# Optimization experiments

Measured on AMD Instinct MI355X. Metric: run time of the kernel, lower is better.

The kernel has to match this reference:

```python
import jax, jax.numpy as jnp
import numpy as np

L = 2048; V = 50000; E = 256
H1 = 512; H2 = 512; H3 = 512; H4 = 512
T = 11; START = 9; STOP = 10; ALPHA = 0.2
NEG = -10000.0


def setup_inputs() -> dict:
    key = jax.random.key(0)
    ks = jax.random.split(key, 25)
    def n(k, shape, s=0.05):
        return jax.random.normal(k, shape, dtype=jnp.float32) * s
    h1 = H1 // 2; h2 = H4 // 2
    trans = jax.random.normal(ks[23], (T, T), dtype=jnp.float32)
    trans = trans.at[START, :].set(NEG).at[:, STOP].set(NEG)
    return {
        "sentence": jax.random.randint(ks[0], (L,), 0, V),
        "emb": n(ks[1], (V, E), 0.1),
        "l1_wih_f": n(ks[2], (4 * h1, E)), "l1_whh_f": n(ks[3], (4 * h1, h1)), "l1_b_f": n(ks[4], (4 * h1,)),
        "l1_wih_b": n(ks[5], (4 * h1, E)), "l1_whh_b": n(ks[6], (4 * h1, h1)), "l1_b_b": n(ks[7], (4 * h1,)),
        "hc1": n(ks[8], (4, h1)),
        "gat1_W": n(ks[9], (H1, H2)), "gat1_a": n(ks[10], (2 * H2,)),
        "gat2_W": n(ks[11], (H2, H3)), "gat2_a": n(ks[12], (2 * H3,)),
        "l2_wih_f": n(ks[13], (4 * h2, H3)), "l2_whh_f": n(ks[14], (4 * h2, h2)), "l2_b_f": n(ks[15], (4 * h2,)),
        "l2_wih_b": n(ks[16], (4 * h2, H3)), "l2_whh_b": n(ks[17], (4 * h2, h2)), "l2_b_b": n(ks[18], (4 * h2,)),
        "hc2": n(ks[19], (4, h2)),
        "w_tag": n(ks[20], (T, H4)), "b_tag": n(ks[21], (T,)),
        "trans": trans,
    }


def _lstm_dir(x, h0, c0, wih, whh, b):
    # x: [L, D]; PyTorch gate order i, f, g, o
    def step(carry, xt):
        h, c = carry
        z = xt @ wih.T + h @ whh.T + b
        i, f, g, o = jnp.split(z, 4)
        i = jax.nn.sigmoid(i); f = jax.nn.sigmoid(f)
        g = jnp.tanh(g); o = jax.nn.sigmoid(o)
        c = f * c + i * g
        h = o * jnp.tanh(c)
        return (h, c), h
    _, hs = jax.lax.scan(step, (h0, c0), x)
    return hs


def _bilstm(x, wf, uf, bf, wb, ub, bb, hc):
    hf = _lstm_dir(x, hc[0], hc[1], wf, uf, bf)
    hb = _lstm_dir(x[::-1], hc[2], hc[3], wb, ub, bb)[::-1]
    return jnp.concatenate([hf, hb], axis=-1)  # [L, 2h]


def _gat(h, W, a):
    # dense GAT layer: attention over all node pairs (inference, no dropout)
    Wh = h @ W                                   # [L, F]
    F = W.shape[1]
    e = jax.nn.leaky_relu((Wh @ a[:F])[:, None] + (Wh @ a[F:])[None, :], ALPHA)  # [L, L]
    attn = jax.nn.softmax(e, axis=1)
    return attn @ Wh


def _viterbi(feats, trans):
    init = jnp.full((T,), NEG, dtype=feats.dtype).at[START].set(0.0)
    def step(fv, feat):
        scores = fv[None, :] + trans             # [next_tag, prev_tag]
        bp = jnp.argmax(scores, axis=1)
        fv2 = jnp.max(scores, axis=1) + feat
        return fv2, bp
    fv, bps = jax.lax.scan(step, init, feats)    # bps: [L, T]
    term = fv + trans[STOP]
    best = jnp.argmax(term)
    score = term[best]
    def back(tag, bp):
        return bp[tag], tag
    _, path = jax.lax.scan(back, best, bps, reverse=True)
    return score, path


def reference(sentence, emb, l1_wih_f, l1_whh_f, l1_b_f, l1_wih_b, l1_whh_b, l1_b_b, hc1,
              gat1_W, gat1_a, gat2_W, gat2_a,
              l2_wih_f, l2_whh_f, l2_b_f, l2_wih_b, l2_whh_b, l2_b_b, hc2,
              w_tag, b_tag, trans):
    x = emb[sentence]                                                  # [L, E]
    h1 = _bilstm(x, l1_wih_f, l1_whh_f, l1_b_f, l1_wih_b, l1_whh_b, l1_b_b, hc1)
    g1 = jax.nn.elu(_gat(h1, gat1_W, gat1_a))
    g2 = jax.nn.elu(_gat(g1, gat2_W, gat2_a))
    h2 = _bilstm(g2, l2_wih_f, l2_whh_f, l2_b_f, l2_wih_b, l2_whh_b, l2_b_b, hc2)
    feats = h2 @ w_tag.T + b_tag                                       # [L, T]
    score, path = _viterbi(feats, trans)
    return score, path
```

## Files before the change

### kernel.cpp

```cpp
#include <hip/hip_runtime.h>
#include <hip/hip_bf16.h>
#include <math.h>

#define SEQL 2048
#define EDIM 256
#define HID 256
#define G4 1024
#define HCAT 512
#define TT 11
#define START_TAG 9
#define STOP_TAG 10
#define NEGV -10000.0f
#define ALPHA_LR 0.2f
#define VCH 64
#define VCS 32
#define NU 16
#define NBLK 16

__device__ __forceinline__ float sigf(float x) { return 1.0f / (1.0f + __expf(-x)); }
__device__ __forceinline__ float tanhfast(float x) { return 2.0f / (1.0f + __expf(-2.0f * x)) - 1.0f; }
__device__ __forceinline__ unsigned int bfp(float f) {
    union { float f; unsigned int u; } c; c.f = f;
    return (c.u + 0x7FFFu + ((c.u >> 16) & 1u)) >> 16;
}
__device__ __forceinline__ float bflo(unsigned int u) { return __uint_as_float(u << 16); }
__device__ __forceinline__ float bfhi(unsigned int u) { return __uint_as_float(u & 0xFFFF0000u); }

__global__ void embed_k(const int* __restrict__ sent, const float* __restrict__ emb,
                        float* __restrict__ x) {
    int idx = blockIdx.x * 256 + threadIdx.x;
    int t = idx >> 8, e = idx & 255;
    x[idx] = emb[(size_t)sent[t] * EDIM + e];
}

__global__ __launch_bounds__(256) void gemm_nt(const float* __restrict__ A,
                                               const float* __restrict__ B,
                                               const float* __restrict__ bias,
                                               float* __restrict__ C,
                                               int M, int N, int K) {
    __shared__ float As[16][68];
    __shared__ float Bs[16][68];
    int tid = threadIdx.x;
    int tx = tid & 15, ty = tid >> 4;
    int m0 = blockIdx.y * 64, n0 = blockIdx.x * 64;
    int lr = tid >> 2;
    int lc = (tid & 3) * 4;
    float acc[4][4] = {};
    for (int k0 = 0; k0 < K; k0 += 16) {
        float4 av = *(const float4*)(A + (size_t)(m0 + lr) * K + k0 + lc);
        float4 bv = make_float4(0.f, 0.f, 0.f, 0.f);
        if (n0 + lr < N) bv = *(const float4*)(B + (size_t)(n0 + lr) * K + k0 + lc);
        As[lc + 0][lr] = av.x; As[lc + 1][lr] = av.y; As[lc + 2][lr] = av.z; As[lc + 3][lr] = av.w;
        Bs[lc + 0][lr] = bv.x; Bs[lc + 1][lr] = bv.y; Bs[lc + 2][lr] = bv.z; Bs[lc + 3][lr] = bv.w;
        __syncthreads();
#pragma unroll
        for (int kk = 0; kk < 16; ++kk) {
            float4 a4 = *(const float4*)&As[kk][ty * 4];
            float4 b4 = *(const float4*)&Bs[kk][tx * 4];
            float aa[4] = {a4.x, a4.y, a4.z, a4.w};
            float bb[4] = {b4.x, b4.y, b4.z, b4.w};
#pragma unroll
            for (int i = 0; i < 4; ++i)
#pragma unroll
                for (int j = 0; j < 4; ++j) acc[i][j] += aa[i] * bb[j];
        }
        __syncthreads();
    }
#pragma unroll
    for (int i = 0; i < 4; ++i) {
        int m = m0 + ty * 4 + i;
#pragma unroll
        for (int j = 0; j < 4; ++j) {
            int n = n0 + tx * 4 + j;
            if (n < N) {
                float v = acc[i][j];
                if (bias) v += bias[n];
                C[(size_t)m * N + n] = v;
            }
        }
    }
}

__global__ __launch_bounds__(256) void gemm_nn(const float* __restrict__ A,
                                               const float* __restrict__ B,
                                               float* __restrict__ C,
                                               const float* __restrict__ rowdiv,
                                               int do_elu, int M, int N, int K) {
    __shared__ float As[16][68];
    __shared__ float Bs[16][68];
    int tid = threadIdx.x;
    int tx = tid & 15, ty = tid >> 4;
    int m0 = blockIdx.y * 64, n0 = blockIdx.x * 64;
    int lr = tid >> 2;
    int lc = (tid & 3) * 4;
    int br = tid >> 4;
    int bc = (tid & 15) * 4;
    float acc[4][4] = {};
    for (int k0 = 0; k0 < K; k0 += 16) {
        float4 av = *(const float4*)(A + (size_t)(m0 + lr) * K + k0 + lc);
        float4 bv = *(const float4*)(B + (size_t)(k0 + br) * N + n0 + bc);
        As[lc + 0][lr] = av.x; As[lc + 1][lr] = av.y; As[lc + 2][lr] = av.z; As[lc + 3][lr] = av.w;
        *(float4*)&Bs[br][bc] = bv;
        __syncthreads();
#pragma unroll
        for (int kk = 0; kk < 16; ++kk) {
            float4 a4 = *(const float4*)&As[kk][ty * 4];
            float4 b4 = *(const float4*)&Bs[kk][tx * 4];
            float aa[4] = {a4.x, a4.y, a4.z, a4.w};
            float bb[4] = {b4.x, b4.y, b4.z, b4.w};
#pragma unroll
            for (int i = 0; i < 4; ++i)
#pragma unroll
                for (int j = 0; j < 4; ++j) acc[i][j] += aa[i] * bb[j];
        }
        __syncthreads();
    }
#pragma unroll
    for (int i = 0; i < 4; ++i) {
        int m = m0 + ty * 4 + i;
        float rd = rowdiv ? rowdiv[m] : 1.0f;
#pragma unroll
        for (int j = 0; j < 4; ++j) {
            int n = n0 + tx * 4 + j;
            float v = acc[i][j];
            if (rowdiv) v /= rd;
            if (do_elu) v = v > 0.f ? v : (__expf(v) - 1.f);
            C[(size_t)m * N + n] = v;
        }
    }
}

__global__ __launch_bounds__(256) void lstm_lds(const float* __restrict__ xin_f,
                                                const float* __restrict__ xin_b,
                                                const float* __restrict__ whh_f,
                                                const float* __restrict__ whh_b,
                                                const float* __restrict__ hc,
                                                float* __restrict__ out,
                                                unsigned int* pubu, int tagbase) {
    int raw = blockIdx.x;
    int lane7 = raw & 7;
    if (lane7 > 1) return;
    int dir = lane7;
    int b = raw >> 3;
    const float* xin = dir ? xin_b : xin_f;
    const float* whh = dir ? whh_b : whh_f;

    int tid = threadIdx.x;

    __shared__ uint4 W4[2048];
    __shared__ __align__(16) float hbuf[256];
    __shared__ float zp[512];

    for (int idx = tid; idx < 2048; idx += 256) {
        int wave = idx >> 9;
        int i = (idx >> 6) & 7;
        int l = idx & 63;
        int towner = wave * 64 + l;
        int rp = towner & 31;
        int k8 = towner >> 5;
        int rloc = 2 * rp + (i >> 2);
        int ii = i & 3;
        int g = rloc >> 4, j = rloc & 15;
        const float* wr = whh + (size_t)(g * HID + b * NU + j) * HID + k8 * 32 + ii * 8;
        uint4 v;
        v.x = bfp(wr[0]) | (bfp(wr[1]) << 16);
        v.y = bfp(wr[2]) | (bfp(wr[3]) << 16);
        v.z = bfp(wr[4]) | (bfp(wr[5]) << 16);
        v.w = bfp(wr[6]) | (bfp(wr[7]) << 16);
        W4[wave * 512 + i * 64 + l] = v;
    }

    if (tid < 256) hbuf[tid] = hc[dir * 512 + tid];
    float c = 0.f;
    float xq0 = 0.f, xq1 = 0.f, xq2 = 0.f, xq3 = 0.f;
    if (tid < 16) {
        c = hc[dir * 512 + 256 + b * NU + tid];
        int t0 = dir ? (SEQL - 1) : 0;
        const float* xr = xin + (size_t)t0 * G4 + b * NU + tid;
        xq0 = xr[0]; xq1 = xr[256]; xq2 = xr[512]; xq3 = xr[768];
    }
    __syncthreads();

    int rp = tid & 31;
    int k8 = tid >> 5;
    int wbase = (tid >> 6) * 512 + (tid & 63);
    const float4* hb4 = (const float4*)hbuf;

    for (int s = 0; s < SEQL; ++s) {
        float acc0 = 0.f, acc1 = 0.f;
#pragma unroll
        for (int i = 0; i < 4; ++i) {
            uint4 w0 = W4[wbase + i * 64];
            uint4 w1 = W4[wbase + (i + 4) * 64];
            float4 hA = hb4[k8 * 8 + i * 2];
            float4 hB = hb4[k8 * 8 + i * 2 + 1];
            acc0 += bflo(w0.x) * hA.x + bfhi(w0.x) * hA.y + bflo(w0.y) * hA.z + bfhi(w0.y) * hA.w
                  + bflo(w0.z) * hB.x + bfhi(w0.z) * hB.y + bflo(w0.w) * hB.z + bfhi(w0.w) * hB.w;
            acc1 += bflo(w1.x) * hA.x + bfhi(w1.x) * hA.y + bflo(w1.y) * hA.z + bfhi(w1.y) * hA.w
                  + bflo(w1.z) * hB.x + bfhi(w1.z) * hB.y + bflo(w1.w) * hB.z + bfhi(w1.w) * hB.w;
        }
        zp[k8 * 64 + 2 * rp] = acc0;
        zp[k8 * 64 + 2 * rp + 1] = acc1;
        __syncthreads();

        int t = dir ? (SEQL - 1 - s) : s;
        int par = (s + 1) & 1;
        unsigned int etag = (unsigned int)(tagbase + s + 1) & 0xFFFFu;
        unsigned int* slot = pubu + (par * 2 + dir) * 256;

        if (tid < 16) {
            float zi = xq0, zf = xq1, zg = xq2, zo = xq3;
#pragma unroll
            for (int q = 0; q < 8; ++q) {
                zi += zp[q * 64 + tid];
                zf += zp[q * 64 + 16 + tid];
                zg += zp[q * 64 + 32 + tid];
                zo += zp[q * 64 + 48 + tid];
            }
            float ig = sigf(zi), fg = sigf(zf), gt = tanhfast(zg), og = sigf(zo);
            c = fg * c + ig * gt;
            float hn = og * tanhfast(c);
            hbuf[b * NU + tid] = hn;
            unsigned int word = (bfp(hn) << 16) | etag;
            int u = b * NU + tid;
            *(volatile unsigned int*)&slot[u] = word;
            __hip_atomic_store(&slot[u], word, __ATOMIC_RELAXED,
                               __HIP_MEMORY_SCOPE_AGENT);
            out[(size_t)t * HCAT + dir * HID + u] = hn;
            if (s + 1 < SEQL) {
                int tn = dir ? (SEQL - 2 - s) : (s + 1);
                const float* xr = xin + (size_t)tn * G4 + b * NU + tid;
                xq0 = xr[0]; xq1 = xr[256]; xq2 = xr[512]; xq3 = xr[768];
            }
        } else if (tid >= 64 && s + 1 < SEQL) {
            int pu = tid - 64;
            int u = pu < b * NU ? pu : pu + NU;
            unsigned int v; int it = 0;
            for (;;) {
                v = *(volatile const unsigned int*)&slot[u];
                if ((v & 0xFFFFu) == etag) break;
                if ((++it & 7) == 0) {
                    v = __hip_atomic_load(&slot[u], __ATOMIC_RELAXED,
                                          __HIP_MEMORY_SCOPE_AGENT);
                    if ((v & 0xFFFFu) == etag) break;
                }
            }
            hbuf[u] = bfhi(v);
            if (pu < 48) {
                int pu2 = pu + 192;
                int u2 = pu2 < b * NU ? pu2 : pu2 + NU;
                it = 0;
                for (;;) {
                    v = *(volatile const unsigned int*)&slot[u2];
                    if ((v & 0xFFFFu) == etag) break;
                    if ((++it & 7) == 0) {
                        v = __hip_atomic_load(&slot[u2], __ATOMIC_RELAXED,
                                              __HIP_MEMORY_SCOPE_AGENT);
                        if ((v & 0xFFFFu) == etag) break;
                    }
                }
                hbuf[u2] = bfhi(v);
            }
        }
        __syncthreads();
    }
}

__global__ void gat_scores(const float* __restrict__ Wh, const float* __restrict__ a,
                           float* __restrict__ s1, float* __restrict__ s2) {
    int i = blockIdx.x;
    int lane = threadIdx.x;
    const float* rowp = Wh + (size_t)i * HCAT;
    float p1 = 0.f, p2 = 0.f;
    for (int k = lane; k < HCAT; k += 64) {
        float w = rowp[k];
        p1 += w * a[k];
        p2 += w * a[HCAT + k];
    }
    for (int off = 32; off; off >>= 1) {
        p1 += __shfl_down(p1, off, 64);
        p2 += __shfl_down(p2, off, 64);
    }
    if (lane == 0) { s1[i] = p1; s2[i] = p2; }
}

__global__ void reduce_max_k(const float* __restrict__ s2, float* __restrict__ outv) {
    __shared__ float red[256];
    int tid = threadIdx.x;
    float m = -INFINITY;
    for (int k = tid; k < SEQL; k += 256) m = fmaxf(m, s2[k]);
    red[tid] = m;
    __syncthreads();
    for (int off = 128; off; off >>= 1) {
        if (tid < off) red[tid] = fmaxf(red[tid], red[tid + off]);
        __syncthreads();
    }
    if (tid == 0) outv[0] = red[0];
}

__global__ void gat_p(const float* __restrict__ s1, const float* __restrict__ s2,
                      const float* __restrict__ s2m, float* __restrict__ P,
                      float* __restrict__ Z) {
    int i = blockIdx.x;
    int tid = threadIdx.x;
    float base = s1[i];
    float m = base + s2m[0];
    m = m > 0.f ? m : ALPHA_LR * m;
    float zs = 0.f;
    for (int jj = tid; jj < SEQL; jj += 256) {
        float e = base + s2[jj];
        e = e > 0.f ? e : ALPHA_LR * e;
        float p = __expf(e - m);
        P[(size_t)i * SEQL + jj] = p;
        zs += p;
    }
    __shared__ float red[256];
    red[tid] = zs;
    __syncthreads();
    for (int off = 128; off; off >>= 1) {
        if (tid < off) red[tid] += red[tid + off];
        __syncthreads();
    }
    if (tid == 0) Z[i] = red[0];
}

__global__ void vit_chunkA(const float* __restrict__ feats, const float* __restrict__ trans,
                           float* __restrict__ chunkA) {
    int c = blockIdx.x;
    int tid = threadIdx.x;
    __shared__ float Acur[121], tr[121];
    if (tid < 121) tr[tid] = trans[tid];
    __syncthreads();
    int n = tid / 11, p = tid % 11;
    int t0 = c * VCS;
    if (tid < 121) Acur[tid] = tr[tid] + feats[t0 * TT + n];
    __syncthreads();
    for (int t = t0 + 1; t < t0 + VCS; ++t) {
        float v = -INFINITY;
        if (tid < 121) {
            float ft = feats[t * TT + n];
#pragma unroll
            for (int k = 0; k < 11; ++k) v = fmaxf(v, tr[n * 11 + k] + Acur[k * 11 + p]);
            v += ft;
        }
        __syncthreads();
        if (tid < 121) Acur[tid] = v;
        __syncthreads();
    }
    if (tid < 121) chunkA[c * 121 + tid] = Acur[tid];
}

__global__ void vit_prefix(const float* __restrict__ chunkA, float* __restrict__ fvstart) {
    int tid = threadIdx.x;
    __shared__ float fv[11];
    if (tid < 11) fv[tid] = (tid == START_TAG) ? 0.f : NEGV;
    __syncthreads();
    if (tid < 11) fvstart[tid] = fv[tid];
    for (int c = 0; c < VCH; ++c) {
        float v = -INFINITY;
        if (tid < 11) {
            for (int p = 0; p < 11; ++p) v = fmaxf(v, chunkA[c * 121 + tid * 11 + p] + fv[p]);
        }
        __syncthreads();
        if (tid < 11) { fv[tid] = v; fvstart[(c + 1) * TT + tid] = v; }
        __syncthreads();
    }
}

__global__ void vit_chunkC(const float* __restrict__ feats, const float* __restrict__ trans,
                           const float* __restrict__ fvstart, int* __restrict__ bp,
                           float* __restrict__ fvfinal) {
    int c = blockIdx.x;
    int tid = threadIdx.x;
    __shared__ float fv[11], tr[121], sc[121], mx[11];
    if (tid < 121) tr[tid] = trans[tid];
    if (tid < 11) fv[tid] = fvstart[c * TT + tid];
    __syncthreads();
    int t0 = c * VCS;
    for (int t = t0; t < t0 + VCS; ++t) {
        if (tid < 121) sc[tid] = fv[tid % 11] + tr[tid];
        __syncthreads();
        if (tid < 11) {
            float best = -INFINITY;
            int bi = 0;
            for (int k = 0; k < 11; ++k) {
                float v = sc[tid * 11 + k];
                if (v > best) { best = v; bi = k; }
            }
            bp[t * TT + tid] = bi;
            mx[tid] = best + feats[t * TT + tid];
        }
        __syncthreads();
        if (tid < 11) fv[tid] = mx[tid];
        __syncthreads();
    }
    if (c == VCH - 1 && tid < 11) fvfinal[tid] = fv[tid];
}

__global__ __launch_bounds__(1024) void vit_back(const int* __restrict__ bp,
                                                 const float* __restrict__ fvfinal,
                                                 const float* __restrict__ trans,
                                                 float* __restrict__ outp) {
    __shared__ unsigned char bufA[SEQL * TT];
    __shared__ unsigned char bufB[SEQL * TT];
    __shared__ int bestIdx;
    int tid = threadIdx.x;
    for (int idx = tid; idx < SEQL * TT; idx += 1024) {
        int t = idx / TT, n = idx - t * TT;
        bufA[idx] = (t < SEQL - 1) ? (unsigned char)bp[(t + 1) * TT + n] : (unsigned char)n;
    }
    __syncthreads();
    unsigned char* a = bufA;
    unsigned char* b = bufB;
    for (int len = 1; len < SEQL - 1; len <<= 1) {
        for (int idx = tid; idx < SEQL * TT; idx += 1024) {
            int t = idx / TT, n = idx - t * TT;
            int m = (t + len <= SEQL - 1) ? (int)a[(t + len) * TT + n] : n;
            b[t * TT + n] = a[t * TT + m];
        }
        __syncthreads();
        unsigned char* tmp = a; a = b; b = tmp;
        __syncthreads();
    }
    if (tid == 0) {
        float bs = -INFINITY;
        int bi = 0;
        for (int p = 0; p < 11; ++p) {
            float v = fvfinal[p] + trans[STOP_TAG * 11 + p];
            if (v > bs) { bs = v; bi = p; }
        }
        outp[0] = bs;
        bestIdx = bi;
    }
    __syncthreads();
    int best = bestIdx;
    for (int t = tid; t < SEQL; t += 1024) outp[1 + t] = (float)a[t * TT + best];
}

extern "C" void kernel_launch(void* const* d_in, const int* in_sizes, int n_in,
                              void* d_out, int out_size, void* d_ws, size_t ws_size,
                              hipStream_t stream) {
    const int* sent = (const int*)d_in[0];
    const float* emb = (const float*)d_in[1];
    const float* w1f = (const float*)d_in[2];
    const float* u1f = (const float*)d_in[3];
    const float* b1f = (const float*)d_in[4];
    const float* w1b = (const float*)d_in[5];
    const float* u1b = (const float*)d_in[6];
    const float* b1b = (const float*)d_in[7];
    const float* hc1 = (const float*)d_in[8];
    const float* g1W = (const float*)d_in[9];
    const float* g1a = (const float*)d_in[10];
    const float* g2W = (const float*)d_in[11];
    const float* g2a = (const float*)d_in[12];
    const float* w2f = (const float*)d_in[13];
    const float* u2f = (const float*)d_in[14];
    const float* b2f = (const float*)d_in[15];
    const float* w2b = (const float*)d_in[16];
    const float* u2b = (const float*)d_in[17];
    const float* b2b = (const float*)d_in[18];
    const float* hc2 = (const float*)d_in[19];
    const float* wtag = (const float*)d_in[20];
    const float* btag = (const float*)d_in[21];
    const float* trans = (const float*)d_in[22];

    float* ws = (float*)d_ws;
    float* x = ws;
    float* R1 = x + 524288;
    float* xin_f = R1;
    float* xin_b = R1 + 2097152;
    float* P = R1;
    float* h1cat = R1 + 4194304;
    float* Wh = h1cat + 1048576;
    float* g1 = Wh + 1048576;
    float* s1 = g1 + 1048576;
    float* s2 = s1 + 2048;
    float* Zr = s2 + 2048;
    float* s2m = Zr + 2048;
    unsigned int* pub = (unsigned int*)(s2m + 16);
    float* feats = (float*)(pub + 1024);
    float* chA = feats + 22528;
    float* fvst = chA + 7744;
    float* fvfin = fvst + 720;
    int* bp = (int*)(fvfin + 16);

    hipMemsetAsync(pub, 0, 1024 * sizeof(unsigned int), stream);

    embed_k<<<SEQL, 256, 0, stream>>>(sent, emb, x);

    gemm_nt<<<dim3(16, 32), 256, 0, stream>>>(x, w1f, b1f, xin_f, SEQL, G4, EDIM);
    gemm_nt<<<dim3(16, 32), 256, 0, stream>>>(x, w1b, b1b, xin_b, SEQL, G4, EDIM);
    lstm_lds<<<128, 256, 0, stream>>>(xin_f, xin_b, u1f, u1b, hc1, h1cat, pub, 0);

    gemm_nn<<<dim3(8, 32), 256, 0, stream>>>(h1cat, g1W, Wh, nullptr, 0, SEQL, HCAT, HCAT);
    gat_scores<<<SEQL, 64, 0, stream>>>(Wh, g1a, s1, s2);
    reduce_max_k<<<1, 256, 0, stream>>>(s2, s2m);
    gat_p<<<SEQL, 256, 0, stream>>>(s1, s2, s2m, P, Zr);
    gemm_nn<<<dim3(8, 32), 256, 0, stream>>>(P, Wh, g1, Zr, 1, SEQL, HCAT, SEQL);

    gemm_nn<<<dim3(8, 32), 256, 0, stream>>>(g1, g2W, Wh, nullptr, 0, SEQL, HCAT, HCAT);
    gat_scores<<<SEQL, 64, 0, stream>>>(Wh, g2a, s1, s2);
    reduce_max_k<<<1, 256, 0, stream>>>(s2, s2m);
    gat_p<<<SEQL, 256, 0, stream>>>(s1, s2, s2m, P, Zr);
    float* g2v = h1cat;
    gemm_nn<<<dim3(8, 32), 256, 0, stream>>>(P, Wh, g2v, Zr, 1, SEQL, HCAT, SEQL);

    gemm_nt<<<dim3(16, 32), 256, 0, stream>>>(g2v, w2f, b2f, xin_f, SEQL, G4, HCAT);
    gemm_nt<<<dim3(16, 32), 256, 0, stream>>>(g2v, w2b, b2b, xin_b, SEQL, G4, HCAT);
    float* h2cat = g1;
    lstm_lds<<<128, 256, 0, stream>>>(xin_f, xin_b, u2f, u2b, hc2, h2cat, pub, 2048);

    gemm_nt<<<dim3(1, 32), 256, 0, stream>>>(h2cat, wtag, btag, feats, SEQL, TT, HCAT);
    vit_chunkA<<<VCH, 128, 0, stream>>>(feats, trans, chA);
    vit_prefix<<<1, 128, 0, stream>>>(chA, fvst);
    vit_chunkC<<<VCH, 128, 0, stream>>>(feats, trans, fvst, bp, fvfin);
    vit_back<<<1, 1024, 0, stream>>>(bp, fvfin, trans, (float*)d_out);
}
```

Measured before the change: 7.900 ms.

## Split-K the GAT GEMMs with separate reduction kernels and adaptive LSTM polling

The GAT GEMMs, previously launched as 256 blocks, now split K four ways across a z-grid so more workgroups run on the many CUs. Partial sums go to a scratch buffer and are reduced by new sum/finalize kernels that also apply the row normalization and ELU. Separately, the LSTM cross-block polling is moved into a helper that switches to atomic-only loads once it sees the volatile read return a stale value. This adds extra memory traffic for the partial buffers plus additional kernel launches.

```diff
diff --git a/kernel.cpp b/kernel.cpp
--- a/kernel.cpp
+++ b/kernel.cpp
@@ -26,6 +26,30 @@
 __device__ __forceinline__ float bflo(unsigned int u) { return __uint_as_float(u << 16); }
 __device__ __forceinline__ float bfhi(unsigned int u) { return __uint_as_float(u & 0xFFFF0000u); }
 
+__device__ __forceinline__ unsigned int poll_word(unsigned int* p, unsigned int etag,
+                                                  int& mode) {
+    unsigned int v;
+    if (mode) {
+        for (;;) {
+            v = __hip_atomic_load(p, __ATOMIC_RELAXED, __HIP_MEMORY_SCOPE_AGENT);
+            if ((v & 0xFFFFu) == etag) return v;
+        }
+    }
+    int it = 0;
+    for (;;) {
+        v = *(volatile const unsigned int*)p;
+        if ((v & 0xFFFFu) == etag) return v;
+        if ((++it & 3) == 0) {
+            v = __hip_atomic_load(p, __ATOMIC_RELAXED, __HIP_MEMORY_SCOPE_AGENT);
+            if ((v & 0xFFFFu) == etag) {
+                unsigned int w = *(volatile const unsigned int*)p;
+                if ((w & 0xFFFFu) != etag) mode = 1;
+                return v;
+            }
+        }
+    }
+}
+
 __global__ void embed_k(const int* __restrict__ sent, const float* __restrict__ emb,
                         float* __restrict__ x) {
     int idx = blockIdx.x * 256 + threadIdx.x;
@@ -81,22 +105,24 @@
     }
 }
 
-__global__ __launch_bounds__(256) void gemm_nn(const float* __restrict__ A,
-                                               const float* __restrict__ B,
-                                               float* __restrict__ C,
-                                               const float* __restrict__ rowdiv,
-                                               int do_elu, int M, int N, int K) {
+__global__ __launch_bounds__(256) void gemm_nn_ks(const float* __restrict__ A,
+                                                  const float* __restrict__ B,
+                                                  float* __restrict__ Cpart,
+                                                  int M, int N, int K4) {
     __shared__ float As[16][68];
     __shared__ float Bs[16][68];
     int tid = threadIdx.x;
     int tx = tid & 15, ty = tid >> 4;
     int m0 = blockIdx.y * 64, n0 = blockIdx.x * 64;
+    int kz = blockIdx.z;
+    int K = (int)gridDim.z * K4;
+    int kbeg = kz * K4, kend = kbeg + K4;
     int lr = tid >> 2;
     int lc = (tid & 3) * 4;
     int br = tid >> 4;
     int bc = (tid & 15) * 4;
     float acc[4][4] = {};
-    for (int k0 = 0; k0 < K; k0 += 16) {
+    for (int k0 = kbeg; k0 < kend; k0 += 16) {
         float4 av = *(const float4*)(A + (size_t)(m0 + lr) * K + k0 + lc);
         float4 bv = *(const float4*)(B + (size_t)(k0 + br) * N + n0 + bc);
         As[lc + 0][lr] = av.x; As[lc + 1][lr] = av.y; As[lc + 2][lr] = av.z; As[lc + 3][lr] = av.w;
@@ -115,19 +141,29 @@
         }
         __syncthreads();
     }
+    float* Cz = Cpart + (size_t)kz * M * N;
 #pragma unroll
     for (int i = 0; i < 4; ++i) {
         int m = m0 + ty * 4 + i;
-        float rd = rowdiv ? rowdiv[m] : 1.0f;
 #pragma unroll
         for (int j = 0; j < 4; ++j) {
             int n = n0 + tx * 4 + j;
-            float v = acc[i][j];
-            if (rowdiv) v /= rd;
-            if (do_elu) v = v > 0.f ? v : (__expf(v) - 1.f);
-            C[(size_t)m * N + n] = v;
-        }
-    }
+            Cz[(size_t)m * N + n] = acc[i][j];
+        }
+    }
+}
+
+__global__ void attn_fin(const float* __restrict__ Cp, const float* __restrict__ Zr,
+                         float* __restrict__ C, int MN, int N) {
+    int idx = blockIdx.x * 256 + threadIdx.x;
+    float v = Cp[idx] + Cp[MN + idx] + Cp[2 * MN + idx] + Cp[3 * MN + idx];
+    v /= Zr[idx / N];
+    C[idx] = v > 0.f ? v : (__expf(v) - 1.f);
+}
+
+__global__ void sum4_fin(const float* __restrict__ Cp, float* __restrict__ C, int MN) {
+    int idx = blockIdx.x * 256 + threadIdx.x;
+    C[idx] = Cp[idx] + Cp[MN + idx] + Cp[2 * MN + idx] + Cp[3 * MN + idx];
 }
 
 __global__ __launch_bounds__(256) void lstm_lds(const float* __restrict__ xin_f,
@@ -186,6 +222,8 @@
     int wbase = (tid >> 6) * 512 + (tid & 63);
     const float4* hb4 = (const float4*)hbuf;
 
+    int mode1 = 0, mode2 = 0;
+
     for (int s = 0; s < SEQL; ++s) {
         float acc0 = 0.f, acc1 = 0.f;
 #pragma unroll
@@ -204,9 +242,8 @@
         __syncthreads();
 
         int t = dir ? (SEQL - 1 - s) : s;
-        int par = (s + 1) & 1;
         unsigned int etag = (unsigned int)(tagbase + s + 1) & 0xFFFFu;
-        unsigned int* slot = pubu + (par * 2 + dir) * 256;
+        unsigned int* slot = pubu + (((s + 1) & 1) * 2 + dir) * 256;
 
         if (tid < 16) {
             float zi = xq0, zf = xq1, zg = xq2, zo = xq3;
@@ -235,30 +272,12 @@
         } else if (tid >= 64 && s + 1 < SEQL) {
             int pu = tid - 64;
             int u = pu < b * NU ? pu : pu + NU;
-            unsigned int v; int it = 0;
-            for (;;) {
-                v = *(volatile const unsigned int*)&slot[u];
-                if ((v & 0xFFFFu) == etag) break;
-                if ((++it & 7) == 0) {
-                    v = __hip_atomic_load(&slot[u], __ATOMIC_RELAXED,
-                                          __HIP_MEMORY_SCOPE_AGENT);
-                    if ((v & 0xFFFFu) == etag) break;
-                }
-            }
+            unsigned int v = poll_word(&slot[u], etag, mode1);
             hbuf[u] = bfhi(v);
             if (pu < 48) {
                 int pu2 = pu + 192;
                 int u2 = pu2 < b * NU ? pu2 : pu2 + NU;
-                it = 0;
-                for (;;) {
-                    v = *(volatile const unsigned int*)&slot[u2];
-                    if ((v & 0xFFFFu) == etag) break;
-                    if ((++it & 7) == 0) {
-                        v = __hip_atomic_load(&slot[u2], __ATOMIC_RELAXED,
-                                              __HIP_MEMORY_SCOPE_AGENT);
-                        if ((v & 0xFFFFu) == etag) break;
-                    }
-                }
+                v = poll_word(&slot[u2], etag, mode2);
                 hbuf[u2] = bfhi(v);
             }
         }
@@ -483,6 +502,7 @@
     float* fvst = chA + 7744;
     float* fvfin = fvst + 720;
     int* bp = (int*)(fvfin + 16);
+    float* Cpart = (float*)(bp + 22528);
 
     hipMemsetAsync(pub, 0, 1024 * sizeof(unsigned int), stream);
 
@@ -492,18 +512,22 @@
     gemm_nt<<<dim3(16, 32), 256, 0, stream>>>(x, w1b, b1b, xin_b, SEQL, G4, EDIM);
     lstm_lds<<<128, 256, 0, stream>>>(xin_f, xin_b, u1f, u1b, hc1, h1cat, pub, 0);
 
-    gemm_nn<<<dim3(8, 32), 256, 0, stream>>>(h1cat, g1W, Wh, nullptr, 0, SEQL, HCAT, HCAT);
+    gemm_nn_ks<<<dim3(8, 32, 4), 256, 0, stream>>>(h1cat, g1W, Cpart, SEQL, HCAT, HCAT / 4);
+    sum4_fin<<<4096, 256, 0, stream>>>(Cpart, Wh, SEQL * HCAT);
     gat_scores<<<SEQL, 64, 0, stream>>>(Wh, g1a, s1, s2);
     reduce_max_k<<<1, 256, 0, stream>>>(s2, s2m);
     gat_p<<<SEQL, 256, 0, stream>>>(s1, s2, s2m, P, Zr);
-    gemm_nn<<<dim3(8, 32), 256, 0, stream>>>(P, Wh, g1, Zr, 1, SEQL, HCAT, SEQL);
-
-    gemm_nn<<<dim3(8, 32), 256, 0, stream>>>(g1, g2W, Wh, nullptr, 0, SEQL, HCAT, HCAT);
+    gemm_nn_ks<<<dim3(8, 32, 4), 256, 0, stream>>>(P, Wh, Cpart, SEQL, HCAT, SEQL / 4);
+    attn_fin<<<4096, 256, 0, stream>>>(Cpart, Zr, g1, SEQL * HCAT, HCAT);
+
+    gemm_nn_ks<<<dim3(8, 32, 4), 256, 0, stream>>>(g1, g2W, Cpart, SEQL, HCAT, HCAT / 4);
+    sum4_fin<<<4096, 256, 0, stream>>>(Cpart, Wh, SEQL * HCAT);
     gat_scores<<<SEQL, 64, 0, stream>>>(Wh, g2a, s1, s2);
     reduce_max_k<<<1, 256, 0, stream>>>(s2, s2m);
     gat_p<<<SEQL, 256, 0, stream>>>(s1, s2, s2m, P, Zr);
     float* g2v = h1cat;
-    gemm_nn<<<dim3(8, 32), 256, 0, stream>>>(P, Wh, g2v, Zr, 1, SEQL, HCAT, SEQL);
+    gemm_nn_ks<<<dim3(8, 32, 4), 256, 0, stream>>>(P, Wh, Cpart, SEQL, HCAT, SEQL / 4);
+    attn_fin<<<4096, 256, 0, stream>>>(Cpart, Zr, g2v, SEQL * HCAT, HCAT);
 
     gemm_nt<<<dim3(16, 32), 256, 0, stream>>>(g2v, w2f, b2f, xin_f, SEQL, G4, HCAT);
     gemm_nt<<<dim3(16, 32), 256, 0, stream>>>(g2v, w2b, b2b, xin_b, SEQL, G4, HCAT);
```

Result: slower. 10.00 ms (+26.6%).
